# Kernel tuning notes

Hardware: AMD Instinct MI355X
Metric: run time of the kernel (lower is better)

Reference implementation:

```python
import jax, jax.numpy as jnp
import numpy as np

NC = 64
W = 64
H = 64
BZ = 2


def _ca_module(fg, mask, p, prop_size):
    """ContextualAttentionModule forward. fg (bz,nc,w,h), mask (bz,1,w,h)."""
    bz, nc, w, h = fg.shape
    pad = p // 2

    def per_sample(fg_b, m_b):  # fg_b (nc,w,h), m_b (1,w,h)
        bg = fg_b * (1.0 - m_b)
        pbg = jnp.pad(bg, ((0, 0), (pad, pad), (pad, pad)))
        # patch kernels: K[(y,x), c, i, j] = pbg[c, y+i, x+j]  (matches torch unfold order)
        shifts = jnp.stack([pbg[:, i:i + w, j:j + h]
                            for i in range(p) for j in range(p)], axis=0)  # (p*p,nc,w,h)
        K = shifts.transpose(2, 3, 1, 0).reshape(w * h, nc, p, p) + 1e-7  # (L,nc,p,p)
        K = K / jnp.sqrt(jnp.sum(K ** 2, axis=(1, 2, 3), keepdims=True))
        # patch-similarity attention: conv2d with L dynamic kernels -> (1,L,w,h)
        scores = jax.lax.conv_general_dilated(
            fg_b[None], K, (1, 1), [(pad, pad), (pad, pad)],
            dimension_numbers=('NCHW', 'OIHW', 'NCHW'))
        if prop_size != 1:
            # grouped conv with ones kernel, padding=1 (as in torch code) == box-sum
            scores = jax.lax.reduce_window(
                scores, 0.0, jax.lax.add,
                (1, 1, prop_size, prop_size), (1, 1, 1, 1),
                [(0, 0), (0, 0), (1, 1), (1, 1)])
        att = jax.nn.softmax(scores, axis=1)
        # conv_transpose2d(att, K, padding=pad) == conv2d with spatially flipped, IO-swapped K
        Kt = jnp.flip(K, (2, 3)).transpose(1, 0, 2, 3)  # (nc,L,p,p)
        rec = jax.lax.conv_general_dilated(
            att, Kt, (1, 1), [(pad, pad), (pad, pad)],
            dimension_numbers=('NCHW', 'OIHW', 'NCHW'))[0]  # (nc,w,h)
        rec = rec * m_b / float(p * p)
        return rec + fg_b * (1.0 - m_b)

    return jax.vmap(per_sample)(fg, mask)


def setup_inputs() -> dict:
    key = jax.random.key(0)
    ks = jax.random.split(key, 8)
    foreground = jax.random.normal(ks[0], (BZ, NC, W, H), dtype=jnp.float32)
    mask = (jax.random.uniform(ks[1], (BZ, 1, W, H)) < 0.25).astype(jnp.float32)
    c2 = 2 * NC  # inchannel * num_of_modules
    # SE module linears (squeeze_ratio=1.0), torch Linear convention: y = x @ W.T + b
    W1 = jax.random.normal(ks[2], (c2, c2), dtype=jnp.float32) / np.sqrt(c2)
    b1 = jnp.zeros((c2,), dtype=jnp.float32)
    W2 = jax.random.normal(ks[3], (c2, c2), dtype=jnp.float32) / np.sqrt(c2)
    b2 = jnp.zeros((c2,), dtype=jnp.float32)
    # combiner 1x1 conv: (out=NC, in=2*NC)
    Wc = jax.random.normal(ks[4], (NC, c2), dtype=jnp.float32) / np.sqrt(c2)
    bc = jnp.zeros((NC,), dtype=jnp.float32)
    return {"foreground": foreground, "mask": mask,
            "W1": W1, "b1": b1, "W2": W2, "b2": b2, "Wc": Wc, "bc": bc}


def reference(foreground, mask, W1, b1, W2, b2, Wc, bc):
    # two parallel contextual-attention branches: (patch=1,prop=3) and (patch=3,prop=3)
    o0 = _ca_module(foreground, mask, 1, 3)
    o1 = _ca_module(foreground, mask, 3, 3)
    outs = jnp.concatenate([o0, o1], axis=1)  # (bz, 2*nc, w, h)
    # SE module: global avg pool -> Linear/ReLU/Linear/Sigmoid -> channel scale
    s = outs.mean(axis=(2, 3))  # (bz, 2*nc)
    g = jax.nn.sigmoid(jax.nn.relu(s @ W1.T + b1) @ W2.T + b2)
    outs = outs * g[:, :, None, None]
    # combiner 1x1 conv
    return jnp.einsum('bchw,oc->bohw', outs, Wc) + bc[None, :, None, None]
```

## Files before the change

### kernel.cpp

```cpp
#include <hip/hip_runtime.h>
#include <math.h>

#define WW 64
#define HH 64
#define L 4096
#define NC 64
#define D3 576
#define ASCALE (1.0f/128.0f)
#define QB 32
#define NSPLIT 4
#define D9W 2200

typedef _Float16 f16x8 __attribute__((ext_vector_type(8)));
typedef _Float16 f16x4 __attribute__((ext_vector_type(4)));
typedef float    f32x4 __attribute__((ext_vector_type(4)));

__device__ __forceinline__ float wave_max(float v){
  #pragma unroll
  for(int o=32;o;o>>=1) v = fmaxf(v, __shfl_xor(v,o));
  return v;
}
__device__ __forceinline__ float wave_sum(float v){
  #pragma unroll
  for(int o=32;o;o>>=1) v += __shfl_xor(v,o);
  return v;
}
__device__ __forceinline__ void gload16(const void* g, void* l){
  __builtin_amdgcn_global_load_lds((const __attribute__((address_space(1))) unsigned int*)g,
                                   (__attribute__((address_space(3))) unsigned int*)l,
                                   16, 0, 0);
}

__global__ __launch_bounds__(256) void prep_fg(const float* __restrict__ fg,
                                               const float* __restrict__ mask,
                                               float* __restrict__ fgT,
                                               _Float16* __restrict__ bgH){
  __shared__ float tile[64][65];
  __shared__ float msh[64];
  const int z = blockIdx.y;
  const int q0 = blockIdx.x*64;
  const int tx = threadIdx.x & 63, ty = threadIdx.x >> 6;
  if(threadIdx.x < 64) msh[threadIdx.x] = mask[(size_t)z*L + q0 + threadIdx.x];
  #pragma unroll
  for(int i=0;i<16;i++){
    const int c = ty*16 + i;
    tile[c][tx] = fg[((size_t)z*64 + c)*L + q0 + tx];
  }
  __syncthreads();
  #pragma unroll
  for(int i=0;i<16;i++){
    const int q = ty*16 + i;
    fgT[((size_t)z*L + q0 + q)*64 + tx] = tile[tx][q];
  }
  const float mval = (1.0f - msh[tx])*128.0f;
  #pragma unroll
  for(int i=0;i<16;i++){
    const int c = ty*16 + i;
    bgH[((size_t)z*64 + c)*L + q0 + tx] = (_Float16)(tile[c][tx]*mval);
  }
}

__global__ __launch_bounds__(256) void build_all(const float* __restrict__ fgT,
                                                 const float* __restrict__ mask,
                                                 _Float16* __restrict__ BhatH1,
                                                 _Float16* __restrict__ PfgH1,
                                                 _Float16* __restrict__ BhatH3,
                                                 _Float16* __restrict__ PfgH3,
                                                 float* __restrict__ rn3){
  const int t = threadIdx.x, c = t & 63, sub = t >> 6;
  const int l = blockIdx.x*4 + sub, z = blockIdx.y;
  const float* fgz = fgT + (size_t)z*L*64;
  const float* mz  = mask + (size_t)z*L;
  const int y = l >> 6, x = l & 63;
  float Wn[5][5];
  #pragma unroll
  for(int u=0;u<5;u++){
    const int yy = y+u-2;
    #pragma unroll
    for(int v=0;v<5;v++){
      const int xx = x+v-2;
      Wn[u][v] = (yy>=0 && yy<HH && xx>=0 && xx<WW) ? fgz[(size_t)(yy*WW+xx)*64 + c] : 0.f;
    }
  }
  float m3[3][3];
  #pragma unroll
  for(int i=0;i<3;i++){
    #pragma unroll
    for(int j=0;j<3;j++){
      const int yy = y+i-1, xx = x+j-1;
      m3[i][j] = (yy>=0&&yy<HH&&xx>=0&&xx<WW) ? mz[yy*WW+xx] : 0.f;
    }
  }
  {
    const float K1 = Wn[2][2]*(1.0f - m3[1][1]) + 1e-7f;
    const float ss = wave_sum(K1*K1);
    BhatH1[((size_t)z*L + l)*NC + c] = (_Float16)(K1*rsqrtf(ss));
    float s = 0.f;
    #pragma unroll
    for(int a=0;a<3;a++)
      #pragma unroll
      for(int b=0;b<3;b++) s += Wn[1+a][1+b];
    PfgH1[((size_t)z*L + l)*NC + c] = (_Float16)s;
  }
  {
    float K[9]; float ss = 0.f;
    #pragma unroll
    for(int i=0;i<3;i++)
      #pragma unroll
      for(int j=0;j<3;j++){
        const float v = Wn[1+i][1+j]*(1.0f - m3[i][j]) + 1e-7f;
        K[i*3+j] = v; ss += v*v;
      }
    ss = wave_sum(ss);
    const float rn = rsqrtf(ss);
    _Float16* outp = BhatH3 + ((size_t)z*L + l)*D3 + c*9;
    #pragma unroll
    for(int k=0;k<9;k++) outp[k] = (_Float16)(K[k]*rn);
    if(c==0) rn3[(size_t)z*L + l] = rn;
  }
  {
    const bool dyok[3] = { y-1>=0, true, y+1<HH };
    const bool dxok[3] = { x-1>=0, true, x+1<WW };
    _Float16* outp = PfgH3 + ((size_t)z*L + l)*D3 + c*9;
    #pragma unroll
    for(int i=0;i<3;i++)
      #pragma unroll
      for(int j=0;j<3;j++){
        float acc = 0.f;
        #pragma unroll
        for(int a=0;a<3;a++){
          if(!dyok[a]) continue;
          #pragma unroll
          for(int b=0;b<3;b++){
            if(!dxok[b]) continue;
            acc += Wn[i+a][j+b];
          }
        }
        outp[i*3+j] = (_Float16)acc;
      }
  }
}

__global__ __launch_bounds__(256) void transpose_h(const ushort* __restrict__ src,
                                                   ushort* __restrict__ dst,
                                                   int C, size_t sSz, size_t sDz){
  __shared__ ushort tile[64][65];
  const int z = blockIdx.z;
  src += z*sSz; dst += z*sDz;
  const int bc = blockIdx.x*64, br = blockIdx.y*64;
  const int tx = threadIdx.x & 15, ty = threadIdx.x >> 4;
  #pragma unroll
  for(int i=0;i<4;i++){
    const ushort4 v = *(const ushort4*)(src + (size_t)(br+ty+16*i)*C + bc + tx*4);
    tile[ty+16*i][tx*4+0] = v.x;
    tile[ty+16*i][tx*4+1] = v.y;
    tile[ty+16*i][tx*4+2] = v.z;
    tile[ty+16*i][tx*4+3] = v.w;
  }
  __syncthreads();
  #pragma unroll
  for(int i=0;i<4;i++){
    ushort4 o;
    o.x = tile[tx*4+0][ty+16*i];
    o.y = tile[tx*4+1][ty+16*i];
    o.z = tile[tx*4+2][ty+16*i];
    o.w = tile[tx*4+3][ty+16*i];
    *(ushort4*)(dst + (size_t)(bc+ty+16*i)*L + br + tx*4) = o;
  }
}

__global__ __launch_bounds__(256) void flash_p1(const _Float16* __restrict__ Q,
                                                const _Float16* __restrict__ Km,
                                                const _Float16* __restrict__ Vt,
                                                _Float16* __restrict__ Op,
                                                float* __restrict__ Ml,
                                                float* __restrict__ Ll){
  __shared__ _Float16 Qs[QB*64];
  __shared__ _Float16 KsA[4][QB*64];
  __shared__ _Float16 VsA[4][64*32];
  __shared__ _Float16 PsA[4][QB*32];
  __shared__ float    FwA[4][QB];
  const int z = blockIdx.z, sp = blockIdx.y, q0 = blockIdx.x*QB;
  const int t = threadIdx.x, lane = t&63, wave = t>>6;
  const int r16 = lane&15, g4 = lane>>4;
  _Float16* Ks = KsA[wave];
  _Float16* Vs = VsA[wave];
  _Float16* Ps = PsA[wave];
  float* Fw = FwA[wave];
  {
    const int row = t>>3, ch = t&7;
    gload16(Q + ((size_t)z*L + q0 + row)*64 + ((ch ^ (row&7))<<3), (char*)Qs + t*16);
  }
  asm volatile("s_waitcnt vmcnt(0)" ::: "memory");
  __syncthreads();

  float Mreg[2] = {-3.0e38f, -3.0e38f};
  float Lreg[2] = {0.f, 0.f};
  f32x4 accO[2][4] = {};

  for(int tt=0; tt<8; ++tt){
    const int lbase = sp*1024 + tt*128 + wave*32;
    #pragma unroll
    for(int u=0;u<4;u++){
      const int row = u*8 + (lane>>3), ch = lane&7;
      gload16(Km + ((size_t)z*L + lbase + row)*64 + ((ch ^ (row&7))<<3),
              (char*)Ks + u*1024 + lane*16);
    }
    #pragma unroll
    for(int u=0;u<4;u++){
      const int cst = u*16 + (lane>>2), slot = lane&3;
      gload16(Vt + ((size_t)z*64 + cst)*L + lbase + ((slot ^ (cst&3))<<3),
              (char*)Vs + u*1024 + lane*16);
    }
    asm volatile("s_waitcnt vmcnt(0)" ::: "memory");
    __builtin_amdgcn_sched_barrier(0);
    f32x4 acc[2][2] = {};
    #pragma unroll
    for(int kk=0;kk<2;kk++){
      f16x8 af[2], bf[2];
      #pragma unroll
      for(int i=0;i<2;i++){
        const int row = i*16 + r16;
        af[i] = *(const f16x8*)((const char*)Ks + (((row<<7) + kk*64 + (g4<<4)) ^ ((row&7)<<4)));
      }
      #pragma unroll
      for(int j=0;j<2;j++){
        const int row = j*16 + r16;
        bf[j] = *(const f16x8*)((const char*)Qs + (((row<<7) + kk*64 + (g4<<4)) ^ ((row&7)<<4)));
      }
      #pragma unroll
      for(int i=0;i<2;i++)
        #pragma unroll
        for(int j=0;j<2;j++)
          acc[i][j] = __builtin_amdgcn_mfma_f32_16x16x32_f16(af[i], bf[j], acc[i][j], 0,0,0);
    }
    float fs[2];
    #pragma unroll
    for(int j=0;j<2;j++){
      float mv = -3.0e38f;
      #pragma unroll
      for(int i=0;i<2;i++)
        #pragma unroll
        for(int r=0;r<4;r++) mv = fmaxf(mv, acc[i][j][r]);
      mv = fmaxf(mv, __shfl_xor(mv, 16));
      mv = fmaxf(mv, __shfl_xor(mv, 32));
      const float mnew = fmaxf(Mreg[j], mv);
      fs[j] = __expf(Mreg[j] - mnew);
      Mreg[j] = mnew;
      float ps = 0.f;
      const int q = j*16 + r16;
      #pragma unroll
      for(int i=0;i<2;i++){
        f16x4 ph;
        #pragma unroll
        for(int r=0;r<4;r++){
          const float p = __expf(acc[i][j][r] - mnew);
          ps += p; ph[r] = (_Float16)p;
        }
        *(f16x4*)((char*)Ps + (q<<6) + ((i*32 + g4*8) ^ ((q&3)<<4))) = ph;
      }
      ps += __shfl_xor(ps, 16);
      ps += __shfl_xor(ps, 32);
      Lreg[j] = Lreg[j]*fs[j] + ps;
    }
    if(g4==0){ Fw[r16] = fs[0]; Fw[16+r16] = fs[1]; }
    #pragma unroll
    for(int qb=0;qb<2;qb++){
      float f4[4];
      #pragma unroll
      for(int r=0;r<4;r++) f4[r] = Fw[qb*16 + g4*4 + r];
      #pragma unroll
      for(int cb=0;cb<4;cb++)
        #pragma unroll
        for(int r=0;r<4;r++) accO[qb][cb][r] *= f4[r];
    }
    #pragma unroll
    for(int qb=0;qb<2;qb++){
      const int qrow = qb*16 + r16;
      const f16x8 af = *(const f16x8*)((const char*)Ps + (qrow<<6) + ((g4<<4) ^ ((qrow&3)<<4)));
      #pragma unroll
      for(int cb=0;cb<4;cb++){
        const int crow = cb*16 + r16;
        const f16x8 bf = *(const f16x8*)((const char*)Vs + (crow<<6) + ((g4<<4) ^ ((crow&3)<<4)));
        accO[qb][cb] = __builtin_amdgcn_mfma_f32_16x16x32_f16(af, bf, accO[qb][cb], 0,0,0);
      }
    }
  }
  const int sidx = (z*NSPLIT + sp)*4 + wave;
  #pragma unroll
  for(int qb=0;qb<2;qb++){
    #pragma unroll
    for(int cb=0;cb<4;cb++){
      #pragma unroll
      for(int r=0;r<4;r++){
        const int ql = qb*16 + g4*4 + r;
        Op[((size_t)sidx*L + q0 + ql)*64 + cb*16 + r16] = (_Float16)accO[qb][cb][r];
      }
    }
  }
  if(g4==0){
    Ml[(size_t)sidx*L + q0 + r16]      = Mreg[0];
    Ml[(size_t)sidx*L + q0 + 16 + r16] = Mreg[1];
    Ll[(size_t)sidx*L + q0 + r16]      = Lreg[0];
    Ll[(size_t)sidx*L + q0 + 16 + r16] = Lreg[1];
  }
}

template<int OM, int KS>
__global__ __launch_bounds__(256, 3) void gemm_h16(const _Float16* __restrict__ A, int lda, size_t sAz,
                                                   const _Float16* __restrict__ B, int ldb, size_t sBz,
                                                   void* __restrict__ C, int ldc, size_t sCz,
                                                   int K, size_t sPart){
  __shared__ _Float16 sh[16384];
  _Float16* As = sh;
  _Float16* Bs = sh + 8192;
  const int zz = blockIdx.z;
  const int z = zz / KS, ks = zz % KS;
  const int Kp = K / KS;
  A += (size_t)z*sAz + (size_t)ks*Kp;
  B += (size_t)z*sBz + (size_t)ks*Kp;
  int bxi = blockIdx.x, byi = blockIdx.y;
  if(OM==2){
    const int i = byi*32 + bxi;
    const int xcd = i & 7, tt = (i >> 3) & 127;
    byi = 8*(xcd & 3) + (tt & 7);
    bxi = 16*(xcd >> 2) + (tt >> 3);
  }
  const int bm = byi*128, bn = bxi*128;
  const int t = threadIdx.x, lane = t & 63, wave = t >> 6;
  const int wr = wave >> 1, wc = wave & 1;
  const int r16 = lane & 15, g4 = lane >> 4;
  const int srow = t >> 3;
  const int schunk = t & 7;
  f32x4 acc[4][4] = {};
  for(int k0=0;k0<Kp;k0+=64){
    #pragma unroll
    for(int u=0;u<4;u++){
      const int rowA = u*32 + srow;
      const int colh = ((schunk ^ (rowA & 7)) << 3);
      gload16(A + (size_t)(bm+rowA)*lda + k0 + colh, (char*)As + u*4096 + wave*1024);
      gload16(B + (size_t)(bn+rowA)*ldb + k0 + colh, (char*)Bs + u*4096 + wave*1024);
    }
    __syncthreads();
    #pragma unroll
    for(int kk=0;kk<2;kk++){
      f16x8 af[4], bf[4];
      #pragma unroll
      for(int i=0;i<4;i++){
        const int row = wr*64 + i*16 + r16;
        const int off = ((row<<7) + kk*64 + (g4<<4)) ^ ((row&7)<<4);
        af[i] = *(const f16x8*)((const char*)As + off);
      }
      #pragma unroll
      for(int j=0;j<4;j++){
        const int row = wc*64 + j*16 + r16;
        const int off = ((row<<7) + kk*64 + (g4<<4)) ^ ((row&7)<<4);
        bf[j] = *(const f16x8*)((const char*)Bs + off);
      }
      #pragma unroll
      for(int i=0;i<4;i++)
        #pragma unroll
        for(int j=0;j<4;j++)
          acc[i][j] = __builtin_amdgcn_mfma_f32_16x16x32_f16(af[i], bf[j], acc[i][j], 0, 0, 0);
    }
    __syncthreads();
  }
  _Float16* Cz = (_Float16*)C + (size_t)z*sCz;
  #pragma unroll
  for(int h=0; h<2; ++h){
    __syncthreads();
    if(wr == h){
      #pragma unroll
      for(int i=0;i<4;i++){
        const int row0 = i*16 + g4*4;
        #pragma unroll
        for(int j=0;j<4;j++){
          const int col = wc*64 + j*16 + r16;
          #pragma unroll
          for(int r=0;r<4;r++)
            sh[(row0+r)*136 + col] = (_Float16)acc[i][j][r];
        }
      }
    }
    __syncthreads();
    #pragma unroll
    for(int k=0;k<4;k++){
      const int row = k*16 + (t>>4);
      const int cg = (t&15)*8;
      const f16x8 v = *(const f16x8*)(sh + row*136 + cg);
      *(f16x8*)(Cz + (size_t)(bm + h*64 + row)*ldc + bn + cg) = v;
    }
  }
}

__global__ __launch_bounds__(256, 3) void gemm_pv64(const _Float16* __restrict__ A,
                                                    const _Float16* __restrict__ B,
                                                    _Float16* __restrict__ C,
                                                    size_t sPart){
  __shared__ _Float16 sh[12288];
  _Float16* As = sh;
  _Float16* Bs = sh + 8192;
  const int zz = blockIdx.z;
  const int z = zz >> 3, ks = zz & 7;
  const int Kp = L/8;
  const _Float16* Az = A + (size_t)z*L*L + (size_t)ks*Kp;
  const _Float16* Bz = B + (size_t)z*64*L + (size_t)ks*Kp;
  const int bm = blockIdx.y*128;
  const int t = threadIdx.x, lane = t&63, wave = t>>6;
  const int r16 = lane&15, g4 = lane>>4;
  const int srow = t>>3, schunk = t&7;
  f32x4 acc[2][4] = {};
  for(int k0=0;k0<Kp;k0+=64){
    #pragma unroll
    for(int u=0;u<4;u++){
      const int rowA = u*32 + srow;
      const int colh = ((schunk ^ (rowA & 7)) << 3);
      gload16(Az + (size_t)(bm+rowA)*L + k0 + colh, (char*)As + u*4096 + wave*1024);
    }
    #pragma unroll
    for(int u=0;u<2;u++){
      const int rowB = u*32 + srow;
      const int colh = ((schunk ^ (rowB & 7)) << 3);
      gload16(Bz + (size_t)rowB*L + k0 + colh, (char*)Bs + u*4096 + wave*1024);
    }
    __syncthreads();
    #pragma unroll
    for(int kk=0;kk<2;kk++){
      f16x8 af[2], bf[4];
      #pragma unroll
      for(int i=0;i<2;i++){
        const int row = wave*32 + i*16 + r16;
        const int off = ((row<<7) + kk*64 + (g4<<4)) ^ ((row&7)<<4);
        af[i] = *(const f16x8*)((const char*)As + off);
      }
      #pragma unroll
      for(int j=0;j<4;j++){
        const int row = j*16 + r16;
        const int off = ((row<<7) + kk*64 + (g4<<4)) ^ ((row&7)<<4);
        bf[j] = *(const f16x8*)((const char*)Bs + off);
      }
      #pragma unroll
      for(int i=0;i<2;i++)
        #pragma unroll
        for(int j=0;j<4;j++)
          acc[i][j] = __builtin_amdgcn_mfma_f32_16x16x32_f16(af[i], bf[j], acc[i][j], 0, 0, 0);
    }
    __syncthreads();
  }
  #pragma unroll
  for(int i=0;i<2;i++){
    const int row0 = wave*32 + i*16 + g4*4;
    #pragma unroll
    for(int j=0;j<4;j++){
      const int col = j*16 + r16;
      #pragma unroll
      for(int r=0;r<4;r++)
        sh[(row0+r)*72 + col] = (_Float16)acc[i][j][r];
    }
  }
  __syncthreads();
  _Float16* Cz = C + (size_t)ks*sPart + (size_t)z*L*64;
  #pragma unroll
  for(int it=0; it<4; ++it){
    const int row = it*32 + (t>>3);
    const int cg = (t&7)*8;
    const f16x8 v = *(const f16x8*)(sh + row*72 + cg);
    *(f16x8*)(Cz + (size_t)(bm+row)*64 + cg) = v;
  }
}

__global__ __launch_bounds__(256) void softmax_rn(_Float16* __restrict__ S,
                                                  const float* __restrict__ rn3,
                                                  float* __restrict__ Tq){
  __shared__ float red[4];
  const int q = blockIdx.x, z = blockIdx.y, t = threadIdx.x;
  _Float16* p = S + ((size_t)z*L + q)*L;
  float v[16];
  {
    const f16x8 a = *(const f16x8*)(p + t*16);
    const f16x8 b = *(const f16x8*)(p + t*16 + 8);
    #pragma unroll
    for(int i=0;i<8;i++){ v[i] = (float)a[i]; v[8+i] = (float)b[i]; }
  }
  float mx = -3.0e38f;
  #pragma unroll
  for(int i=0;i<16;i++) mx = fmaxf(mx, v[i]);
  mx = wave_max(mx);
  if((t&63)==0) red[t>>6]=mx;
  __syncthreads();
  mx = fmaxf(fmaxf(red[0],red[1]), fmaxf(red[2],red[3]));
  __syncthreads();
  float s = 0.f;
  #pragma unroll
  for(int i=0;i<16;i++){ v[i] = __expf(v[i]-mx); s += v[i]; }
  s = wave_sum(s);
  if((t&63)==0) red[t>>6]=s;
  __syncthreads();
  s = red[0]+red[1]+red[2]+red[3];
  __syncthreads();
  const float inv = 1.0f/s;
  const float* rnz = rn3 + (size_t)z*L + t*16;
  float T = 0.f;
  f16x8 a, b;
  #pragma unroll
  for(int i=0;i<8;i++){
    const float w0 = v[i]*inv*rnz[i];
    const float w1 = v[8+i]*inv*rnz[8+i];
    T += w0 + w1;
    a[i] = (_Float16)(w0*ASCALE);
    b[i] = (_Float16)(w1*ASCALE);
  }
  *(f16x8*)(p + t*16) = a;
  *(f16x8*)(p + t*16 + 8) = b;
  T = wave_sum(T);
  if((t&63)==0) red[t>>6]=T;
  __syncthreads();
  if(t==0) Tq[(size_t)z*L + q] = red[0]+red[1]+red[2]+red[3];
}

__global__ __launch_bounds__(256) void d9_pass(const _Float16* __restrict__ in,
                                               _Float16* __restrict__ out){
  __shared__ _Float16 rows[9*D9W];
  const int bx = blockIdx.x, by = blockIdx.y, t = threadIdx.x;
  const int a = (bx&7)*512 + (bx>>3);
  const int z = by & 1, h = by >> 1;
  const int cbase = h*2048 - 72;
  const int ya = a>>6, xa = a&63;
  const int DY[9] = {-1,-1,-1, 0,0,0, 1,1,1};
  const int DX[9] = {-1, 0, 1,-1,0,1,-1,0,1};
  bool vr[9];
  #pragma unroll
  for(int k=0;k<9;k++){
    const int yy = ya + DY[k], xx = xa + DX[k];
    vr[k] = (yy>=0 && yy<64 && xx>=0 && xx<64);
    if(vr[k]){
      const _Float16* src = in + ((size_t)z*L + a + DY[k]*64 + DX[k])*L;
      int g0 = cbase + t*8;
      g0 = g0 < 0 ? 0 : g0;
      gload16(src + g0, (char*)rows + k*(D9W*2) + t*16);
      const int g1 = cbase + (256+t)*8;
      if(t < 18 && g1 < L)
        gload16(src + g1, (char*)rows + k*(D9W*2) + 4096 + t*16);
    }
  }
  __syncthreads();
  const int m0 = h*2048 + t*8;
  const int ym = m0>>6, x0 = m0&63;
  float o[8] = {0,0,0,0,0,0,0,0};
  #pragma unroll
  for(int k=0;k<9;k++){
    const int D = DY[k]*64 + DX[k];
    const bool vy = vr[k] && ((unsigned)(ym + DY[k]) < 64u);
    if(!vy) continue;
    const int r = ((D % 8) + 8) % 8;
    const int loff = t*8 + 72 + D - r;
    const _Float16* p = rows + k*D9W + loff;
    _Float16 buf[16];
    *(f16x8*)(buf)   = *(const f16x8*)(p);
    *(f16x8*)(buf+8) = *(const f16x8*)(p+8);
    #pragma unroll
    for(int i=0;i<8;i++){
      const bool vx = (unsigned)(x0 + i + DX[k]) < 64u;
      o[i] += vx ? (float)buf[r + i] : 0.f;
    }
  }
  f16x8 w0;
  #pragma unroll
  for(int i=0;i<8;i++) w0[i] = (_Float16)o[i];
  *(f16x8*)(out + ((size_t)z*L + a)*L + m0) = w0;
}

__global__ __launch_bounds__(256) void epilogue_qc(const _Float16* __restrict__ Op,
                                                   const float* __restrict__ Ml,
                                                   const float* __restrict__ Ll,
                                                   const _Float16* __restrict__ Cp,
                                                   const float* __restrict__ Tq,
                                                   const float* __restrict__ fgT,
                                                   const float* __restrict__ mask,
                                                   float* __restrict__ outs,
                                                   float* __restrict__ part,
                                                   size_t sPart){
  __shared__ float ps[4][128];
  const int z = blockIdx.y, t = threadIdx.x;
  const int sub = t >> 6;
  const int q = blockIdx.x*4 + sub, c = t & 63;
  const float m = mask[(size_t)z*L + q];
  const float f = fgT[((size_t)z*L + q)*64 + c];
  float o1, o3;
  {
    float mv[16];
    float ms = -3.0e38f;
    #pragma unroll
    for(int s=0;s<16;s++){
      mv[s] = Ml[(size_t)(z*16+s)*L + q];
      ms = fmaxf(ms, mv[s]);
    }
    float acc = 0.f, Lt = 0.f;
    #pragma unroll
    for(int s=0;s<16;s++){
      const float w0 = __expf(mv[s] - ms);
      acc += w0 * (float)Op[((size_t)(z*16+s)*L + q)*64 + c];
      Lt  += w0 * Ll[(size_t)(z*16+s)*L + q];
    }
    const float o = acc/Lt;
    o1 = o*m + f*(1.0f-m);
    outs[((size_t)z*L + q)*128 + c] = o1;
  }
  {
    const int y = q >> 6, x = q & 63;
    const size_t idx = ((size_t)z*L + q)*64 + c;
    float rec = 0.f;
    #pragma unroll
    for(int k=0;k<8;k++) rec += (float)Cp[(size_t)k*sPart + idx];
    float tb = 0.f;
    #pragma unroll
    for(int dy=-1;dy<=1;dy++){
      const int yy = y+dy;
      if(yy<0||yy>=64) continue;
      #pragma unroll
      for(int dx=-1;dx<=1;dx++){
        const int xx = x+dx;
        if(xx<0||xx>=64) continue;
        tb += Tq[(size_t)z*L + yy*64+xx];
      }
    }
    rec += 1e-7f*tb;
    o3 = rec*(m*(1.0f/9.0f)) + f*(1.0f-m);
    outs[((size_t)z*L + q)*128 + 64 + c] = o3;
  }
  ps[sub][c] = o1;
  ps[sub][64 + c] = o3;
  __syncthreads();
  if(t < 128){
    const float s = ps[0][t] + ps[1][t] + ps[2][t] + ps[3][t];
    part[((size_t)z*1024 + blockIdx.x)*128 + t] = s;
  }
}

__global__ __launch_bounds__(512) void se_mlp(const float* __restrict__ part,
                                              const float* __restrict__ W1, const float* __restrict__ b1,
                                              const float* __restrict__ W2, const float* __restrict__ b2,
                                              float* __restrict__ g){
  __shared__ float red[4][128];
  __shared__ float s[128], h[128];
  const int z = blockIdx.x, t = threadIdx.x;
  const int ch = t & 127, sl = t >> 7;
  float a0 = 0.f;
  for(int j=sl*256; j<(sl+1)*256; ++j)
    a0 += part[((size_t)z*1024 + j)*128 + ch];
  red[sl][ch] = a0;
  __syncthreads();
  if(t < 128) s[t] = (red[0][t]+red[1][t]+red[2][t]+red[3][t])*(1.0f/4096.0f);
  __syncthreads();
  if(t < 128){
    float a = b1[t];
    const float* w = W1 + (size_t)t*128;
    for(int j=0;j<128;j++) a = fmaf(w[j], s[j], a);
    h[t] = fmaxf(a, 0.f);
  }
  __syncthreads();
  if(t < 128){
    float o = b2[t];
    const float* w = W2 + (size_t)t*128;
    for(int j=0;j<128;j++) o = fmaf(w[j], h[j], o);
    g[z*128+t] = 1.0f/(1.0f + __expf(-o));
  }
}

__global__ __launch_bounds__(256) void combiner(const float* __restrict__ outs,
                                                const float* __restrict__ g,
                                                const float* __restrict__ Wc,
                                                const float* __restrict__ bc,
                                                float* __restrict__ out){
  __shared__ float sc[128][33];
  const int z = blockIdx.y, q0 = blockIdx.x*32, t = threadIdx.x;
  const float* gz = g + z*128;
  #pragma unroll
  for(int it=0; it<4; ++it){
    const int qi = it*8 + (t>>5);
    const int c4 = (t&31)*4;
    const float4 v = *(const float4*)(outs + ((size_t)z*L + q0 + qi)*128 + c4);
    sc[c4+0][qi] = v.x*gz[c4+0];
    sc[c4+1][qi] = v.y*gz[c4+1];
    sc[c4+2][qi] = v.z*gz[c4+2];
    sc[c4+3][qi] = v.w*gz[c4+3];
  }
  __syncthreads();
  const int qi = t & 31, ob = t >> 5;
  float acc[8];
  #pragma unroll
  for(int k=0;k<8;k++) acc[k] = bc[ob*8+k];
  for(int ch=0; ch<128; ++ch){
    const float v = sc[ch][qi];
    #pragma unroll
    for(int k=0;k<8;k++)
      acc[k] = fmaf(v, Wc[(size_t)(ob*8+k)*128 + ch], acc[k]);
  }
  #pragma unroll
  for(int k=0;k<8;k++){
    const int o = ob*8 + k;
    out[((size_t)z*64 + o)*L + q0 + qi] = acc[k];
  }
}

extern "C" void kernel_launch(void* const* d_in, const int* in_sizes, int n_in,
                              void* d_out, int out_size, void* d_ws, size_t ws_size,
                              hipStream_t stream){
  const float* fg   = (const float*)d_in[0];
  const float* mask = (const float*)d_in[1];
  const float* W1   = (const float*)d_in[2];
  const float* b1   = (const float*)d_in[3];
  const float* W2   = (const float*)d_in[4];
  const float* b2   = (const float*)d_in[5];
  const float* Wc   = (const float*)d_in[6];
  const float* bc   = (const float*)d_in[7];
  float* out = (float*)d_out;

  char* w = (char*)d_ws;
  size_t off = 0;
  auto alloc = [&](size_t bytes)->void*{
    void* p = (void*)(w + off);
    off += (bytes + 255) & ~(size_t)255;
    return p;
  };
  _Float16* S    = (_Float16*)alloc(2ull*L*L*2);
  _Float16* DxB  = (_Float16*)alloc(2ull*L*L*2);
  _Float16* Cp16 = (_Float16*)alloc(8ull*2*L*64*2);
  float* outs  = (float*)alloc(2ull*L*128*4);
  float* fgT   = (float*)alloc(2ull*L*64*4);
  _Float16* BhatH1 = (_Float16*)alloc(2ull*L*64*2);
  _Float16* BhatT1 = (_Float16*)alloc(2ull*64*L*2);
  _Float16* PfgH1  = (_Float16*)alloc(2ull*L*64*2);
  _Float16* BhatH3 = (_Float16*)alloc(2ull*L*D3*2);
  _Float16* PfgH3  = (_Float16*)alloc(2ull*L*D3*2);
  _Float16* bgH    = (_Float16*)alloc(2ull*64*L*2);
  _Float16* Opb = (_Float16*)alloc((size_t)32*L*64*2);
  float* Mlb  = (float*)alloc((size_t)32*L*4);
  float* Llb  = (float*)alloc((size_t)32*L*4);
  float* rn3v = (float*)alloc(2ull*L*4);
  float* Tq   = (float*)alloc(2ull*L*4);
  float* part = (float*)alloc(2ull*1024*128*4);
  float* gbuf = (float*)alloc(1024);
  const size_t sPart = 2ull*L*64;

  prep_fg<<<dim3(64,2),256,0,stream>>>(fg, mask, fgT, bgH);
  build_all<<<dim3(L/4,2),256,0,stream>>>(fgT, mask, BhatH1, PfgH1, BhatH3, PfgH3, rn3v);
  transpose_h<<<dim3(1,64,2),256,0,stream>>>((const ushort*)BhatH1, (ushort*)BhatT1,
                                             64, (size_t)L*64, (size_t)64*L);

  flash_p1<<<dim3(L/QB,NSPLIT,2),256,0,stream>>>(PfgH1, BhatH1, BhatT1, Opb, Mlb, Llb);

  gemm_h16<2,1><<<dim3(32,32,2),256,0,stream>>>(
      PfgH3, D3, (size_t)L*D3,
      BhatH3, D3, (size_t)L*D3,
      (void*)S, L, (size_t)L*L, D3, 0);
  softmax_rn<<<dim3(L,2),256,0,stream>>>(S, rn3v, Tq);
  d9_pass<<<dim3(L,4),256,0,stream>>>(S, DxB);
  gemm_pv64<<<dim3(1,32,16),256,0,stream>>>(DxB, bgH, Cp16, sPart);

  epilogue_qc<<<dim3(L/4,2),256,0,stream>>>(Opb, Mlb, Llb, Cp16, Tq, fgT, mask,
                                            outs, part, sPart);

  se_mlp<<<2,512,0,stream>>>(part, W1, b1, W2, b2, gbuf);
  combiner<<<dim3(L/32,2),256,0,stream>>>(outs, gbuf, Wc, bc, out);
}
```

Baseline: 218.3 us.

## Process two adjacent output rows per block in d9_pass and transpose 3x3 patch layout

d9_pass now handles two horizontally adjacent attention rows per block. The 12 shared neighbour rows are loaded once instead of 2x9, so global traffic on the large score matrix drops by about a third, at the cost of more shared memory per block and half as many blocks. Separately, build_all now writes BhatH3 and PfgH3 in tap-major order (k*64+c) rather than channel-major (c*9+k). This makes the stores coalesced across lanes, and because both GEMM operands are permuted the same way the dot products are unchanged.

```diff
diff --git a/kernel.cpp b/kernel.cpp
--- a/kernel.cpp
+++ b/kernel.cpp
@@ -113,15 +113,15 @@
       }
     ss = wave_sum(ss);
     const float rn = rsqrtf(ss);
-    _Float16* outp = BhatH3 + ((size_t)z*L + l)*D3 + c*9;
-    #pragma unroll
-    for(int k=0;k<9;k++) outp[k] = (_Float16)(K[k]*rn);
+    _Float16* outp = BhatH3 + ((size_t)z*L + l)*D3;
+    #pragma unroll
+    for(int k=0;k<9;k++) outp[k*64 + c] = (_Float16)(K[k]*rn);
     if(c==0) rn3[(size_t)z*L + l] = rn;
   }
   {
     const bool dyok[3] = { y-1>=0, true, y+1<HH };
     const bool dxok[3] = { x-1>=0, true, x+1<WW };
-    _Float16* outp = PfgH3 + ((size_t)z*L + l)*D3 + c*9;
+    _Float16* outp = PfgH3 + ((size_t)z*L + l)*D3;
     #pragma unroll
     for(int i=0;i<3;i++)
       #pragma unroll
@@ -136,7 +136,7 @@
             acc += Wn[i+a][j+b];
           }
         }
-        outp[i*3+j] = (_Float16)acc;
+        outp[(i*3+j)*64 + c] = (_Float16)acc;
       }
   }
 }
@@ -520,54 +520,70 @@
 
 __global__ __launch_bounds__(256) void d9_pass(const _Float16* __restrict__ in,
                                                _Float16* __restrict__ out){
-  __shared__ _Float16 rows[9*D9W];
+  __shared__ _Float16 rows[12*D9W];
   const int bx = blockIdx.x, by = blockIdx.y, t = threadIdx.x;
-  const int a = (bx&7)*512 + (bx>>3);
+  const int p = (bx&7)*256 + (bx>>3);
+  const int a0 = p*2;
   const int z = by & 1, h = by >> 1;
   const int cbase = h*2048 - 72;
-  const int ya = a>>6, xa = a&63;
+  const int ya = a0>>6, xa = a0&63;
   const int DY[9] = {-1,-1,-1, 0,0,0, 1,1,1};
   const int DX[9] = {-1, 0, 1,-1,0,1,-1,0,1};
-  bool vr[9];
-  #pragma unroll
-  for(int k=0;k<9;k++){
-    const int yy = ya + DY[k], xx = xa + DX[k];
-    vr[k] = (yy>=0 && yy<64 && xx>=0 && xx<64);
-    if(vr[k]){
-      const _Float16* src = in + ((size_t)z*L + a + DY[k]*64 + DX[k])*L;
+  const int BJ[9] = {0,1,2, 4,5,6, 8,9,10};
+  const int DD[12] = {-65,-64,-63,-62, -1,0,1,2, 63,64,65,66};
+  bool vr[2][9];
+  bool ld[12];
+  #pragma unroll
+  for(int j=0;j<12;j++) ld[j] = false;
+  #pragma unroll
+  for(int o=0;o<2;o++){
+    #pragma unroll
+    for(int k=0;k<9;k++){
+      const int yy = ya + DY[k], xx = xa + o + DX[k];
+      vr[o][k] = (yy>=0 && yy<64 && xx>=0 && xx<64);
+      if(vr[o][k]) ld[BJ[k]+o] = true;
+    }
+  }
+  #pragma unroll
+  for(int j=0;j<12;j++){
+    if(ld[j]){
+      const _Float16* src = in + ((size_t)z*L + a0 + DD[j])*L;
       int g0 = cbase + t*8;
       g0 = g0 < 0 ? 0 : g0;
-      gload16(src + g0, (char*)rows + k*(D9W*2) + t*16);
+      gload16(src + g0, (char*)rows + j*(D9W*2) + t*16);
       const int g1 = cbase + (256+t)*8;
       if(t < 18 && g1 < L)
-        gload16(src + g1, (char*)rows + k*(D9W*2) + 4096 + t*16);
+        gload16(src + g1, (char*)rows + j*(D9W*2) + 4096 + t*16);
     }
   }
   __syncthreads();
   const int m0 = h*2048 + t*8;
   const int ym = m0>>6, x0 = m0&63;
-  float o[8] = {0,0,0,0,0,0,0,0};
-  #pragma unroll
-  for(int k=0;k<9;k++){
-    const int D = DY[k]*64 + DX[k];
-    const bool vy = vr[k] && ((unsigned)(ym + DY[k]) < 64u);
-    if(!vy) continue;
-    const int r = ((D % 8) + 8) % 8;
-    const int loff = t*8 + 72 + D - r;
-    const _Float16* p = rows + k*D9W + loff;
-    _Float16 buf[16];
-    *(f16x8*)(buf)   = *(const f16x8*)(p);
-    *(f16x8*)(buf+8) = *(const f16x8*)(p+8);
-    #pragma unroll
-    for(int i=0;i<8;i++){
-      const bool vx = (unsigned)(x0 + i + DX[k]) < 64u;
-      o[i] += vx ? (float)buf[r + i] : 0.f;
-    }
-  }
-  f16x8 w0;
-  #pragma unroll
-  for(int i=0;i<8;i++) w0[i] = (_Float16)o[i];
-  *(f16x8*)(out + ((size_t)z*L + a)*L + m0) = w0;
+  #pragma unroll
+  for(int o=0;o<2;o++){
+    float acc[8] = {0,0,0,0,0,0,0,0};
+    #pragma unroll
+    for(int k=0;k<9;k++){
+      const int D = DY[k]*64 + DX[k];
+      const bool vy = vr[o][k] && ((unsigned)(ym + DY[k]) < 64u);
+      if(!vy) continue;
+      const int r = ((D % 8) + 8) % 8;
+      const int loff = t*8 + 72 + D - r;
+      const _Float16* pp = rows + (BJ[k]+o)*D9W + loff;
+      _Float16 buf[16];
+      *(f16x8*)(buf)   = *(const f16x8*)(pp);
+      *(f16x8*)(buf+8) = *(const f16x8*)(pp+8);
+      #pragma unroll
+      for(int i=0;i<8;i++){
+        const bool vx = (unsigned)(x0 + i + DX[k]) < 64u;
+        acc[i] += vx ? (float)buf[r + i] : 0.f;
+      }
+    }
+    f16x8 w0;
+    #pragma unroll
+    for(int i=0;i<8;i++) w0[i] = (_Float16)acc[i];
+    *(f16x8*)(out + ((size_t)z*L + a0 + o)*L + m0) = w0;
+  }
 }
 
 __global__ __launch_bounds__(256) void epilogue_qc(const _Float16* __restrict__ Op,
@@ -755,7 +771,7 @@
       BhatH3, D3, (size_t)L*D3,
       (void*)S, L, (size_t)L*L, D3, 0);
   softmax_rn<<<dim3(L,2),256,0,stream>>>(S, rn3v, Tq);
-  d9_pass<<<dim3(L,4),256,0,stream>>>(S, DxB);
+  d9_pass<<<dim3(L/2,4),256,0,stream>>>(S, DxB);
   gemm_pv64<<<dim3(1,32,16),256,0,stream>>>(DxB, bgH, Cp16, sPart);
 
   epilogue_qc<<<dim3(L/4,2),256,0,stream>>>(Opb, Mlb, Llb, Cp16, Tq, fgT, mask,
```

Result: faster. 210.4 us (-3.6%).
